# Kernel tuning notes

Hardware: AMD Instinct MI355X
Metric: run time of the kernel (lower is better)

The kernel has to match this reference:

```python
import jax, jax.numpy as jnp
import numpy as np

B, T, D_IN, UNITS = 64, 512, 1024, 1024


def setup_inputs() -> dict:
    key = jax.random.key(0)
    k1, k2, k3 = jax.random.split(key, 3)
    x = jax.random.normal(k1, (B, T, D_IN), dtype=jnp.float32)
    kernel = jax.random.normal(k2, (D_IN, UNITS), dtype=jnp.float32) * (1.0 / np.sqrt(D_IN))
    recurrent_kernel = jax.random.normal(k3, (UNITS, UNITS), dtype=jnp.float32) * (1.0 / np.sqrt(UNITS))
    return {"x": x, "kernel": kernel, "recurrent_kernel": recurrent_kernel}


def reference(x, kernel, recurrent_kernel):
    # Hoist input-to-hidden projection out of the time loop: [B,T,U]
    xk = jnp.einsum('btd,du->btu', x, kernel)

    def step(h, xk_t):
        # Elman step: h' = relu(x_t @ W + h @ U)
        h_new = jax.nn.relu(xk_t + h @ recurrent_kernel)
        return h_new, h_new

    h0 = jnp.zeros((x.shape[0], kernel.shape[1]), dtype=x.dtype)
    _, outs = jax.lax.scan(step, h0, jnp.swapaxes(xk, 0, 1))  # outs: [T,B,U]
    return jnp.swapaxes(outs, 0, 1)  # [B,T,U]
```

## Files before the change

kernel.cpp:

```cpp
#include <hip/hip_runtime.h>
#include <cstdint>
#include <cstddef>


typedef __attribute__((ext_vector_type(8))) short short8;
typedef __attribute__((ext_vector_type(4))) float f32x4;

static __device__ __forceinline__ unsigned short f2bf_rne(float f) {
  unsigned u = __float_as_uint(f);
  u += 0x7fffu + ((u >> 16) & 1u);
  return (unsigned short)(u >> 16);
}

static __device__ __forceinline__ void st_g16_cc(unsigned short* p, unsigned short val) {
  unsigned v32 = val;
  asm volatile("global_store_short %0, %1, off sc0 sc1"
               :: "v"(p), "v"(v32) : "memory");
}
static __device__ __forceinline__ void wait_vm0() {
  asm volatile("s_waitcnt vmcnt(0)" ::: "memory");
}
static __device__ __forceinline__ unsigned ld_flag_cc(const unsigned int* p) {
  unsigned v;
  asm volatile("global_load_dword %0, %1, off sc0 sc1\n\t"
               "s_waitcnt vmcnt(0)"
               : "=v"(v) : "v"(p) : "memory");
  return v;
}
static __device__ __forceinline__ void flag_add_cc(unsigned int* p, unsigned val) {
  asm volatile("global_atomic_add %0, %1, off sc1"
               :: "v"(p), "v"(val) : "memory");
}

__global__ __launch_bounds__(256) void xproj_kernel(const float* __restrict__ x,
                                                    const float* __restrict__ kern,
                                                    float* __restrict__ out) {
  __shared__ unsigned short Abuf[128 * 40];
  __shared__ unsigned short Bbuf[128 * 40];
  const int tid = threadIdx.x;
  const int lane = tid & 63;
  const int wv = tid >> 6;
  const int q = lane >> 4;
  const int lr = lane & 15;
  const int wm = (wv >> 1) * 64;
  const int wn = (wv & 1) * 64;
  const long rowbase = (long)blockIdx.y * 128;
  const int colbase = blockIdx.x * 128;

  f32x4 acc[4][4];
#pragma unroll
  for (int i = 0; i < 4; i++)
#pragma unroll
    for (int j = 0; j < 4; j++) acc[i][j] = (f32x4)0.f;

  for (int kb = 0; kb < 1024; kb += 32) {
#pragma unroll
    for (int r = 0; r < 4; ++r) {
      int idx = tid + r * 256;
      int m = idx >> 3;
      int kk = (idx & 7) * 4;
      float4 v = *(const float4*)(x + (rowbase + m) * 1024 + kb + kk);
      ushort4 w4;
      w4.x = f2bf_rne(v.x); w4.y = f2bf_rne(v.y);
      w4.z = f2bf_rne(v.z); w4.w = f2bf_rne(v.w);
      *(ushort4*)&Abuf[m * 40 + kk] = w4;
    }
#pragma unroll
    for (int r = 0; r < 4; ++r) {
      int idx = tid + r * 256;
      int kr = idx >> 5;
      int nn = (idx & 31) * 4;
      float4 v = *(const float4*)(kern + (long)(kb + kr) * 1024 + colbase + nn);
      Bbuf[(nn + 0) * 40 + kr] = f2bf_rne(v.x);
      Bbuf[(nn + 1) * 40 + kr] = f2bf_rne(v.y);
      Bbuf[(nn + 2) * 40 + kr] = f2bf_rne(v.z);
      Bbuf[(nn + 3) * 40 + kr] = f2bf_rne(v.w);
    }
    __syncthreads();
    short8 af[4], bfr[4];
#pragma unroll
    for (int i = 0; i < 4; i++)
      af[i] = *(const short8*)&Abuf[(wm + i * 16 + lr) * 40 + q * 8];
#pragma unroll
    for (int j = 0; j < 4; j++)
      bfr[j] = *(const short8*)&Bbuf[(wn + j * 16 + lr) * 40 + q * 8];
#pragma unroll
    for (int i = 0; i < 4; i++)
#pragma unroll
      for (int j = 0; j < 4; j++)
        acc[i][j] = __builtin_amdgcn_mfma_f32_16x16x32_bf16(af[i], bfr[j], acc[i][j], 0, 0, 0);
    __syncthreads();
  }
#pragma unroll
  for (int i = 0; i < 4; i++) {
#pragma unroll
    for (int r = 0; r < 4; r++) {
      long row = rowbase + wm + i * 16 + q * 4 + r;
      float* op = out + row * 1024 + colbase + wn + lr;
#pragma unroll
      for (int j = 0; j < 4; j++) op[j * 16] = acc[i][j][r];
    }
  }
}

__global__ __launch_bounds__(256) void rnn_scan_kernel(const float* __restrict__ R,
                                                       float* __restrict__ out,
                                                       unsigned short* __restrict__ hbuf,
                                                       unsigned int* __restrict__ flags) {
  const int tid = threadIdx.x;
  const int lane = tid & 63;
  const int wv = tid >> 6;
  const int q = lane >> 4;
  const int lr = lane & 15;
  const int cluster = blockIdx.x & 3;
  const int cg = blockIdx.x >> 2;

  short8 w[2][8];
#pragma unroll
  for (int nt = 0; nt < 2; nt++) {
    int col = cg * 32 + nt * 16 + lr;
#pragma unroll
    for (int cc = 0; cc < 8; cc++) {
      int k0 = wv * 256 + cc * 32 + q * 8;
      short8 t8;
#pragma unroll
      for (int j = 0; j < 8; j++)
        t8[j] = (short)f2bf_rne(R[(long)(k0 + j) * 1024 + col]);
      w[nt][cc] = t8;
    }
  }

  __shared__ float red[4 * 2 * 64 * 4];
  unsigned int* myflag = flags + cluster * 64;
  const int m_lo = tid >> 5;
  const int myn = tid & 31;
  const int off0 = (wv * 32 + q) * 128 + lr * 8;

  for (int t = 0; t < 512; ++t) {
    f32x4 acc0 = (f32x4)0.f, acc1 = (f32x4)0.f;
    if (t > 0) {
      const unsigned short* hb = hbuf + (size_t)((((t - 1) & 1) * 2 + 0) * 4 + cluster) * 16384;
      const unsigned short* lb = hbuf + (size_t)((((t - 1) & 1) * 2 + 1) * 4 + cluster) * 16384;
      const unsigned short* a0 = hb + off0;
      const unsigned short* a4 = a0 + 2048;
      const unsigned short* b0 = lb + off0;
      const unsigned short* b4 = b0 + 2048;
      short8 ah[8], al[8];
      asm volatile(
          "global_load_dwordx4 %0,  %16, off sc0 sc1\n\t"
          "global_load_dwordx4 %1,  %16, off offset:1024 sc0 sc1\n\t"
          "global_load_dwordx4 %2,  %16, off offset:2048 sc0 sc1\n\t"
          "global_load_dwordx4 %3,  %16, off offset:3072 sc0 sc1\n\t"
          "global_load_dwordx4 %4,  %17, off sc0 sc1\n\t"
          "global_load_dwordx4 %5,  %17, off offset:1024 sc0 sc1\n\t"
          "global_load_dwordx4 %6,  %17, off offset:2048 sc0 sc1\n\t"
          "global_load_dwordx4 %7,  %17, off offset:3072 sc0 sc1\n\t"
          "global_load_dwordx4 %8,  %18, off sc0 sc1\n\t"
          "global_load_dwordx4 %9,  %18, off offset:1024 sc0 sc1\n\t"
          "global_load_dwordx4 %10, %18, off offset:2048 sc0 sc1\n\t"
          "global_load_dwordx4 %11, %18, off offset:3072 sc0 sc1\n\t"
          "global_load_dwordx4 %12, %19, off sc0 sc1\n\t"
          "global_load_dwordx4 %13, %19, off offset:1024 sc0 sc1\n\t"
          "global_load_dwordx4 %14, %19, off offset:2048 sc0 sc1\n\t"
          "global_load_dwordx4 %15, %19, off offset:3072 sc0 sc1\n\t"
          "s_waitcnt vmcnt(0)"
          : "=&v"(ah[0]), "=&v"(ah[1]), "=&v"(ah[2]), "=&v"(ah[3]),
            "=&v"(ah[4]), "=&v"(ah[5]), "=&v"(ah[6]), "=&v"(ah[7]),
            "=&v"(al[0]), "=&v"(al[1]), "=&v"(al[2]), "=&v"(al[3]),
            "=&v"(al[4]), "=&v"(al[5]), "=&v"(al[6]), "=&v"(al[7])
          : "v"(a0), "v"(a4), "v"(b0), "v"(b4)
          : "memory");
#pragma unroll
      for (int cc = 0; cc < 8; cc++) {
        acc0 = __builtin_amdgcn_mfma_f32_16x16x32_bf16(ah[cc], w[0][cc], acc0, 0, 0, 0);
        acc0 = __builtin_amdgcn_mfma_f32_16x16x32_bf16(al[cc], w[0][cc], acc0, 0, 0, 0);
        acc1 = __builtin_amdgcn_mfma_f32_16x16x32_bf16(ah[cc], w[1][cc], acc1, 0, 0, 0);
        acc1 = __builtin_amdgcn_mfma_f32_16x16x32_bf16(al[cc], w[1][cc], acc1, 0, 0, 0);
      }
    }
    *(f32x4*)&red[((wv * 2 + 0) * 64 + lane) * 4] = acc0;
    *(f32x4*)&red[((wv * 2 + 1) * 64 + lane) * 4] = acc1;
    __syncthreads();
#pragma unroll
    for (int mi = 0; mi < 2; ++mi) {
      int m = m_lo + mi * 8;
      int nt = myn >> 4;
      int ln = (myn & 15) + ((m >> 2) & 3) * 16;
      int r = m & 3;
      float s = red[((0 * 2 + nt) * 64 + ln) * 4 + r] + red[((1 * 2 + nt) * 64 + ln) * 4 + r] +
                red[((2 * 2 + nt) * 64 + ln) * 4 + r] + red[((3 * 2 + nt) * 64 + ln) * 4 + r];
      long orow = (long)(cluster * 16 + m) * 512 + t;
      float* op = out + orow * 1024 + cg * 32 + myn;
      float h = s + *op;
      h = fmaxf(h, 0.0f);
      *op = h;
      unsigned short hi = f2bf_rne(h);
      float hf = __uint_as_float(((unsigned)hi) << 16);
      unsigned short lo = f2bf_rne(h - hf);
      int k = cg * 32 + myn;
      int off = (k >> 3) * 128 + m * 8 + (k & 7);
      st_g16_cc(hbuf + (size_t)(((t & 1) * 2 + 0) * 4 + cluster) * 16384 + off, hi);
      st_g16_cc(hbuf + (size_t)(((t & 1) * 2 + 1) * 4 + cluster) * 16384 + off, lo);
    }
    if (t < 511) {
      wait_vm0();
      __syncthreads();
      if (tid == 0) {
        flag_add_cc(myflag, 1u);
        unsigned target = 32u * (unsigned)(t + 1);
        while (ld_flag_cc(myflag) < target) {
          __builtin_amdgcn_s_sleep(1);
        }
      }
      __syncthreads();
    }
  }
}

extern "C" void kernel_launch(void* const* d_in, const int* in_sizes, int n_in,
                              void* d_out, int out_size, void* d_ws, size_t ws_size,
                              hipStream_t stream) {
  const float* x = (const float*)d_in[0];
  const float* kern = (const float*)d_in[1];
  const float* R = (const float*)d_in[2];
  float* out = (float*)d_out;

  unsigned short* hbuf = (unsigned short*)d_ws;
  unsigned int* flags = (unsigned int*)((char*)d_ws + (size_t)2 * 2 * 4 * 16384 * sizeof(unsigned short));
  hipMemsetAsync(flags, 0, 1024, stream);

  dim3 g1(8, 256), b1(256);
  xproj_kernel<<<g1, b1, 0, stream>>>(x, kern, out);
  rnn_scan_kernel<<<128, 256, 0, stream>>>(R, out, hbuf, flags);
}
```

Before: 2.287 ms.

## Restructure recurrent scan into 32 wide blocks with per-wave flag barrier

The scan kernel now launches 32 blocks of 512 threads, each owning 128 output columns with 8 waves splitting K, instead of 128 blocks of 256 threads. The single atomic-counter barrier becomes per-wave monotonic flag stores, polled by a whole wave through a ballot, so waves no longer serialize on thread 0 and two __syncthreads. It also prefetches the xk value, packs the hidden-state stores into 64-bit writes, and overlaps the low-part loads with the high-part MFMAs. The costs are a larger 8-way LDS reduction, more weight registers per thread, and correctness that depends on the flag ordering.

After: 5.029 ms. 120% more time.

```diff
diff --git a/kernel.cpp b/kernel.cpp
--- a/kernel.cpp
+++ b/kernel.cpp
@@ -12,11 +12,6 @@
   return (unsigned short)(u >> 16);
 }
 
-static __device__ __forceinline__ void st_g16_cc(unsigned short* p, unsigned short val) {
-  unsigned v32 = val;
-  asm volatile("global_store_short %0, %1, off sc0 sc1"
-               :: "v"(p), "v"(v32) : "memory");
-}
 static __device__ __forceinline__ void wait_vm0() {
   asm volatile("s_waitcnt vmcnt(0)" ::: "memory");
 }
@@ -27,9 +22,13 @@
                : "=v"(v) : "v"(p) : "memory");
   return v;
 }
-static __device__ __forceinline__ void flag_add_cc(unsigned int* p, unsigned val) {
-  asm volatile("global_atomic_add %0, %1, off sc1"
-               :: "v"(p), "v"(val) : "memory");
+static __device__ __forceinline__ void st_flag_cc(unsigned int* p, unsigned v) {
+  asm volatile("global_store_dword %0, %1, off sc0 sc1"
+               :: "v"(p), "v"(v) : "memory");
+}
+static __device__ __forceinline__ void st_g64_cc(unsigned short* p, unsigned long long v) {
+  asm volatile("global_store_dwordx2 %0, %1, off sc0 sc1"
+               :: "v"(p), "v"(v) : "memory");
 }
 
 __global__ __launch_bounds__(256) void xproj_kernel(const float* __restrict__ x,
@@ -103,10 +102,10 @@
   }
 }
 
-__global__ __launch_bounds__(256) void rnn_scan_kernel(const float* __restrict__ R,
-                                                       float* __restrict__ out,
-                                                       unsigned short* __restrict__ hbuf,
-                                                       unsigned int* __restrict__ flags) {
+__global__ __launch_bounds__(512, 2) void rnn_scan_kernel(const float* __restrict__ R,
+                                                          float* __restrict__ out,
+                                                          unsigned short* __restrict__ hbuf,
+                                                          unsigned int* __restrict__ flags) {
   const int tid = threadIdx.x;
   const int lane = tid & 63;
   const int wv = tid >> 6;
@@ -114,14 +113,15 @@
   const int lr = lane & 15;
   const int cluster = blockIdx.x & 3;
   const int cg = blockIdx.x >> 2;
-
-  short8 w[2][8];
-#pragma unroll
-  for (int nt = 0; nt < 2; nt++) {
-    int col = cg * 32 + nt * 16 + lr;
-#pragma unroll
-    for (int cc = 0; cc < 8; cc++) {
-      int k0 = wv * 256 + cc * 32 + q * 8;
+  const int colbase = cg * 128;
+
+  short8 w[8][4];
+#pragma unroll
+  for (int nt = 0; nt < 8; nt++) {
+    const int col = colbase + nt * 16 + lr;
+#pragma unroll
+    for (int cc = 0; cc < 4; cc++) {
+      const int k0 = wv * 128 + cc * 32 + q * 8;
       short8 t8;
 #pragma unroll
       for (int j = 0; j < 8; j++)
@@ -130,90 +130,96 @@
     }
   }
 
-  __shared__ float red[4 * 2 * 64 * 4];
-  unsigned int* myflag = flags + cluster * 64;
-  const int m_lo = tid >> 5;
-  const int myn = tid & 31;
-  const int off0 = (wv * 32 + q) * 128 + lr * 8;
+  __shared__ float red[8 * 8 * 64 * 4];
+
+  const int m = tid >> 5;
+  const int cw0 = (tid & 31) * 4;
+  const int kglob = colbase + cw0;
+  const int hoff = (kglob >> 3) * 128 + m * 8 + (kglob & 7);
+  const int off0 = (wv * 16 + q) * 128 + lr * 8;
+  const int ntr = cw0 >> 4;
+  const int Lb = (cw0 & 15) + ((m >> 2) << 4);
+  const int rr = m & 3;
+
+  unsigned int* myflags = flags + cluster * 64;
+  unsigned int* myflag = myflags + cg * 8 + wv;
+  float* myout = out + ((long)(cluster * 16 + m) * 512) * 1024 + kglob;
 
   for (int t = 0; t < 512; ++t) {
-    f32x4 acc0 = (f32x4)0.f, acc1 = (f32x4)0.f;
+    const float4 xkv = *(const float4*)(myout + (long)t * 1024);
+    f32x4 acc[8];
+#pragma unroll
+    for (int nt = 0; nt < 8; nt++) acc[nt] = (f32x4)0.f;
+
     if (t > 0) {
-      const unsigned short* hb = hbuf + (size_t)((((t - 1) & 1) * 2 + 0) * 4 + cluster) * 16384;
-      const unsigned short* lb = hbuf + (size_t)((((t - 1) & 1) * 2 + 1) * 4 + cluster) * 16384;
-      const unsigned short* a0 = hb + off0;
-      const unsigned short* a4 = a0 + 2048;
-      const unsigned short* b0 = lb + off0;
-      const unsigned short* b4 = b0 + 2048;
-      short8 ah[8], al[8];
+      const unsigned target = (unsigned)t;
+      unsigned f = ld_flag_cc(myflags + lane);
+      while (__ballot(f < target) != 0ull) {
+        f = ld_flag_cc(myflags + lane);
+      }
+      const unsigned short* a0 =
+          hbuf + (size_t)((((t - 1) & 1) * 2 + 0) * 4 + cluster) * 16384 + off0;
+      const unsigned short* b0 =
+          hbuf + (size_t)((((t - 1) & 1) * 2 + 1) * 4 + cluster) * 16384 + off0;
+      short8 ah[4], al[4];
       asm volatile(
-          "global_load_dwordx4 %0,  %16, off sc0 sc1\n\t"
-          "global_load_dwordx4 %1,  %16, off offset:1024 sc0 sc1\n\t"
-          "global_load_dwordx4 %2,  %16, off offset:2048 sc0 sc1\n\t"
-          "global_load_dwordx4 %3,  %16, off offset:3072 sc0 sc1\n\t"
-          "global_load_dwordx4 %4,  %17, off sc0 sc1\n\t"
-          "global_load_dwordx4 %5,  %17, off offset:1024 sc0 sc1\n\t"
-          "global_load_dwordx4 %6,  %17, off offset:2048 sc0 sc1\n\t"
-          "global_load_dwordx4 %7,  %17, off offset:3072 sc0 sc1\n\t"
-          "global_load_dwordx4 %8,  %18, off sc0 sc1\n\t"
-          "global_load_dwordx4 %9,  %18, off offset:1024 sc0 sc1\n\t"
-          "global_load_dwordx4 %10, %18, off offset:2048 sc0 sc1\n\t"
-          "global_load_dwordx4 %11, %18, off offset:3072 sc0 sc1\n\t"
-          "global_load_dwordx4 %12, %19, off sc0 sc1\n\t"
-          "global_load_dwordx4 %13, %19, off offset:1024 sc0 sc1\n\t"
-          "global_load_dwordx4 %14, %19, off offset:2048 sc0 sc1\n\t"
-          "global_load_dwordx4 %15, %19, off offset:3072 sc0 sc1\n\t"
-          "s_waitcnt vmcnt(0)"
+          "global_load_dwordx4 %0, %8, off sc0 sc1\n\t"
+          "global_load_dwordx4 %1, %8, off offset:1024 sc0 sc1\n\t"
+          "global_load_dwordx4 %2, %8, off offset:2048 sc0 sc1\n\t"
+          "global_load_dwordx4 %3, %8, off offset:3072 sc0 sc1\n\t"
+          "global_load_dwordx4 %4, %9, off sc0 sc1\n\t"
+          "global_load_dwordx4 %5, %9, off offset:1024 sc0 sc1\n\t"
+          "global_load_dwordx4 %6, %9, off offset:2048 sc0 sc1\n\t"
+          "global_load_dwordx4 %7, %9, off offset:3072 sc0 sc1\n\t"
+          "s_waitcnt vmcnt(4)"
           : "=&v"(ah[0]), "=&v"(ah[1]), "=&v"(ah[2]), "=&v"(ah[3]),
-            "=&v"(ah[4]), "=&v"(ah[5]), "=&v"(ah[6]), "=&v"(ah[7]),
-            "=&v"(al[0]), "=&v"(al[1]), "=&v"(al[2]), "=&v"(al[3]),
-            "=&v"(al[4]), "=&v"(al[5]), "=&v"(al[6]), "=&v"(al[7])
-          : "v"(a0), "v"(a4), "v"(b0), "v"(b4)
+            "=&v"(al[0]), "=&v"(al[1]), "=&v"(al[2]), "=&v"(al[3])
+          : "v"(a0), "v"(b0)
           : "memory");
 #pragma unroll
-      for (int cc = 0; cc < 8; cc++) {
-        acc0 = __builtin_amdgcn_mfma_f32_16x16x32_bf16(ah[cc], w[0][cc], acc0, 0, 0, 0);
-        acc0 = __builtin_amdgcn_mfma_f32_16x16x32_bf16(al[cc], w[0][cc], acc0, 0, 0, 0);
-        acc1 = __builtin_amdgcn_mfma_f32_16x16x32_bf16(ah[cc], w[1][cc], acc1, 0, 0, 0);
-        acc1 = __builtin_amdgcn_mfma_f32_16x16x32_bf16(al[cc], w[1][cc], acc1, 0, 0, 0);
-      }
-    }
-    *(f32x4*)&red[((wv * 2 + 0) * 64 + lane) * 4] = acc0;
-    *(f32x4*)&red[((wv * 2 + 1) * 64 + lane) * 4] = acc1;
+      for (int cc = 0; cc < 4; cc++)
+#pragma unroll
+        for (int nt = 0; nt < 8; nt++)
+          acc[nt] = __builtin_amdgcn_mfma_f32_16x16x32_bf16(ah[cc], w[nt][cc], acc[nt], 0, 0, 0);
+      asm volatile("s_waitcnt vmcnt(0)"
+                   : "+v"(al[0]), "+v"(al[1]), "+v"(al[2]), "+v"(al[3])
+                   :: "memory");
+#pragma unroll
+      for (int cc = 0; cc < 4; cc++)
+#pragma unroll
+        for (int nt = 0; nt < 8; nt++)
+          acc[nt] = __builtin_amdgcn_mfma_f32_16x16x32_bf16(al[cc], w[nt][cc], acc[nt], 0, 0, 0);
+    }
+
+#pragma unroll
+    for (int nt = 0; nt < 8; nt++)
+      *(f32x4*)&red[((wv * 8 + nt) * 64 + lane) * 4] = acc[nt];
     __syncthreads();
-#pragma unroll
-    for (int mi = 0; mi < 2; ++mi) {
-      int m = m_lo + mi * 8;
-      int nt = myn >> 4;
-      int ln = (myn & 15) + ((m >> 2) & 3) * 16;
-      int r = m & 3;
-      float s = red[((0 * 2 + nt) * 64 + ln) * 4 + r] + red[((1 * 2 + nt) * 64 + ln) * 4 + r] +
-                red[((2 * 2 + nt) * 64 + ln) * 4 + r] + red[((3 * 2 + nt) * 64 + ln) * 4 + r];
-      long orow = (long)(cluster * 16 + m) * 512 + t;
-      float* op = out + orow * 1024 + cg * 32 + myn;
-      float h = s + *op;
-      h = fmaxf(h, 0.0f);
-      *op = h;
+
+    const float xarr[4] = {xkv.x, xkv.y, xkv.z, xkv.w};
+    float hv[4];
+    unsigned long long hpk = 0ull, lpk = 0ull;
+#pragma unroll
+    for (int j = 0; j < 4; ++j) {
+      float s = 0.f;
+#pragma unroll
+      for (int kq = 0; kq < 8; ++kq)
+        s += red[((kq * 8 + ntr) * 64 + Lb + j) * 4 + rr];
+      float h = fmaxf(s + xarr[j], 0.0f);
+      hv[j] = h;
       unsigned short hi = f2bf_rne(h);
       float hf = __uint_as_float(((unsigned)hi) << 16);
       unsigned short lo = f2bf_rne(h - hf);
-      int k = cg * 32 + myn;
-      int off = (k >> 3) * 128 + m * 8 + (k & 7);
-      st_g16_cc(hbuf + (size_t)(((t & 1) * 2 + 0) * 4 + cluster) * 16384 + off, hi);
-      st_g16_cc(hbuf + (size_t)(((t & 1) * 2 + 1) * 4 + cluster) * 16384 + off, lo);
-    }
-    if (t < 511) {
-      wait_vm0();
-      __syncthreads();
-      if (tid == 0) {
-        flag_add_cc(myflag, 1u);
-        unsigned target = 32u * (unsigned)(t + 1);
-        while (ld_flag_cc(myflag) < target) {
-          __builtin_amdgcn_s_sleep(1);
-        }
-      }
-      __syncthreads();
-    }
+      hpk |= (unsigned long long)hi << (16 * j);
+      lpk |= (unsigned long long)lo << (16 * j);
+    }
+    st_g64_cc(hbuf + (size_t)(((t & 1) * 2 + 0) * 4 + cluster) * 16384 + hoff, hpk);
+    st_g64_cc(hbuf + (size_t)(((t & 1) * 2 + 1) * 4 + cluster) * 16384 + hoff, lpk);
+    wait_vm0();
+    if (lane == 0) st_flag_cc(myflag, (unsigned)(t + 1));
+    float4 hq;
+    hq.x = hv[0]; hq.y = hv[1]; hq.z = hv[2]; hq.w = hv[3];
+    *(float4*)(myout + (long)t * 1024) = hq;
   }
 }
 
@@ -231,5 +237,5 @@
 
   dim3 g1(8, 256), b1(256);
   xproj_kernel<<<g1, b1, 0, stream>>>(x, kern, out);
-  rnn_scan_kernel<<<128, 256, 0, stream>>>(R, out, hbuf, flags);
-}
+  rnn_scan_kernel<<<32, 512, 0, stream>>>(R, out, hbuf, flags);
+}
```

## Replace atomic flag barrier with tag-embedded data polling and fewer larger scan blocks

Applied to the files above, without the earlier changes.

Removes the per-step global atomic counter barrier. Consumers now spin-load the hidden-state buffer until the sign bits of the bf16 hi words match an expected step tag, so the data itself acts as the ready signal. The scan uses 32 blocks of 512 threads, each owning 128 columns, instead of 128 blocks of 256. This cuts the number of participants per cluster and lets each block write packed 16-byte hi/lo units. The tag lives in the sign bit of the hi bf16, which is valid only because ReLU outputs are non-negative. Polling re-reads the whole tile and relies on the visibility order of the 16-byte stores.

Measured after the change: 2.401 ms. 5.0% more time.

```diff
diff --git a/kernel.cpp b/kernel.cpp
--- a/kernel.cpp
+++ b/kernel.cpp
@@ -5,31 +5,12 @@
 
 typedef __attribute__((ext_vector_type(8))) short short8;
 typedef __attribute__((ext_vector_type(4))) float f32x4;
+typedef __attribute__((ext_vector_type(4))) unsigned int u32x4;
 
 static __device__ __forceinline__ unsigned short f2bf_rne(float f) {
   unsigned u = __float_as_uint(f);
   u += 0x7fffu + ((u >> 16) & 1u);
   return (unsigned short)(u >> 16);
-}
-
-static __device__ __forceinline__ void st_g16_cc(unsigned short* p, unsigned short val) {
-  unsigned v32 = val;
-  asm volatile("global_store_short %0, %1, off sc0 sc1"
-               :: "v"(p), "v"(v32) : "memory");
-}
-static __device__ __forceinline__ void wait_vm0() {
-  asm volatile("s_waitcnt vmcnt(0)" ::: "memory");
-}
-static __device__ __forceinline__ unsigned ld_flag_cc(const unsigned int* p) {
-  unsigned v;
-  asm volatile("global_load_dword %0, %1, off sc0 sc1\n\t"
-               "s_waitcnt vmcnt(0)"
-               : "=v"(v) : "v"(p) : "memory");
-  return v;
-}
-static __device__ __forceinline__ void flag_add_cc(unsigned int* p, unsigned val) {
-  asm volatile("global_atomic_add %0, %1, off sc1"
-               :: "v"(p), "v"(val) : "memory");
 }
 
 __global__ __launch_bounds__(256) void xproj_kernel(const float* __restrict__ x,
@@ -103,10 +84,9 @@
   }
 }
 
-__global__ __launch_bounds__(256) void rnn_scan_kernel(const float* __restrict__ R,
-                                                       float* __restrict__ out,
-                                                       unsigned short* __restrict__ hbuf,
-                                                       unsigned int* __restrict__ flags) {
+__global__ __launch_bounds__(512, 2) void rnn_scan_kernel(const float* __restrict__ R,
+                                                          float* __restrict__ out,
+                                                          unsigned char* __restrict__ hbuf) {
   const int tid = threadIdx.x;
   const int lane = tid & 63;
   const int wv = tid >> 6;
@@ -114,14 +94,17 @@
   const int lr = lane & 15;
   const int cluster = blockIdx.x & 3;
   const int cg = blockIdx.x >> 2;
-
-  short8 w[2][8];
-#pragma unroll
-  for (int nt = 0; nt < 2; nt++) {
-    int col = cg * 32 + nt * 16 + lr;
+  const int ks = wv & 3;
+  const int nh = wv >> 2;
+  const int colbase = cg * 128;
+
+  short8 w[4][8];
+#pragma unroll
+  for (int nt = 0; nt < 4; nt++) {
+    const int col = colbase + nh * 64 + nt * 16 + lr;
 #pragma unroll
     for (int cc = 0; cc < 8; cc++) {
-      int k0 = wv * 256 + cc * 32 + q * 8;
+      const int k0 = ks * 256 + cc * 32 + q * 8;
       short8 t8;
 #pragma unroll
       for (int j = 0; j < 8; j++)
@@ -130,90 +113,137 @@
     }
   }
 
-  __shared__ float red[4 * 2 * 64 * 4];
-  unsigned int* myflag = flags + cluster * 64;
-  const int m_lo = tid >> 5;
-  const int myn = tid & 31;
-  const int off0 = (wv * 32 + q) * 128 + lr * 8;
+  __shared__ float red[32 * 264];
+  __shared__ float xbuf[16 * 132];
+
+  const int nw = tid & 127;
+  const int mg = tid >> 7;
+  const int kglob = colbase + nw;
+  const int ntr = nw >> 4;
+  const int rlane = mg * 16 + (nw & 15);
+  const int pm = tid & 15;
+  const int pkq = tid >> 4;
+  const size_t punit = (size_t)((cg * 32 + pkq) * 16 + pm) * 16;
+  const size_t cbase = (size_t)ks * 16384 + q * 512 + lr * 16;
+
+  float* opb0 = out + ((long)(cluster * 16 + mg * 4 + 0) * 512) * 1024 + kglob;
+  float* opb1 = out + ((long)(cluster * 16 + mg * 4 + 1) * 512) * 1024 + kglob;
+  float* opb2 = out + ((long)(cluster * 16 + mg * 4 + 2) * 512) * 1024 + kglob;
+  float* opb3 = out + ((long)(cluster * 16 + mg * 4 + 3) * 512) * 1024 + kglob;
 
   for (int t = 0; t < 512; ++t) {
-    f32x4 acc0 = (f32x4)0.f, acc1 = (f32x4)0.f;
+    const long tOff = (long)t * 1024;
+    const float xk0 = opb0[tOff];
+    const float xk1 = opb1[tOff];
+    const float xk2 = opb2[tOff];
+    const float xk3 = opb3[tOff];
+
+    f32x4 acc[4];
+#pragma unroll
+    for (int nt = 0; nt < 4; nt++) acc[nt] = (f32x4)0.f;
+
     if (t > 0) {
-      const unsigned short* hb = hbuf + (size_t)((((t - 1) & 1) * 2 + 0) * 4 + cluster) * 16384;
-      const unsigned short* lb = hbuf + (size_t)((((t - 1) & 1) * 2 + 1) * 4 + cluster) * 16384;
-      const unsigned short* a0 = hb + off0;
-      const unsigned short* a4 = a0 + 2048;
-      const unsigned short* b0 = lb + off0;
-      const unsigned short* b4 = b0 + 2048;
-      short8 ah[8], al[8];
-      asm volatile(
-          "global_load_dwordx4 %0,  %16, off sc0 sc1\n\t"
-          "global_load_dwordx4 %1,  %16, off offset:1024 sc0 sc1\n\t"
-          "global_load_dwordx4 %2,  %16, off offset:2048 sc0 sc1\n\t"
-          "global_load_dwordx4 %3,  %16, off offset:3072 sc0 sc1\n\t"
-          "global_load_dwordx4 %4,  %17, off sc0 sc1\n\t"
-          "global_load_dwordx4 %5,  %17, off offset:1024 sc0 sc1\n\t"
-          "global_load_dwordx4 %6,  %17, off offset:2048 sc0 sc1\n\t"
-          "global_load_dwordx4 %7,  %17, off offset:3072 sc0 sc1\n\t"
-          "global_load_dwordx4 %8,  %18, off sc0 sc1\n\t"
-          "global_load_dwordx4 %9,  %18, off offset:1024 sc0 sc1\n\t"
-          "global_load_dwordx4 %10, %18, off offset:2048 sc0 sc1\n\t"
-          "global_load_dwordx4 %11, %18, off offset:3072 sc0 sc1\n\t"
-          "global_load_dwordx4 %12, %19, off sc0 sc1\n\t"
-          "global_load_dwordx4 %13, %19, off offset:1024 sc0 sc1\n\t"
-          "global_load_dwordx4 %14, %19, off offset:2048 sc0 sc1\n\t"
-          "global_load_dwordx4 %15, %19, off offset:3072 sc0 sc1\n\t"
-          "s_waitcnt vmcnt(0)"
-          : "=&v"(ah[0]), "=&v"(ah[1]), "=&v"(ah[2]), "=&v"(ah[3]),
-            "=&v"(ah[4]), "=&v"(ah[5]), "=&v"(ah[6]), "=&v"(ah[7]),
-            "=&v"(al[0]), "=&v"(al[1]), "=&v"(al[2]), "=&v"(al[3]),
-            "=&v"(al[4]), "=&v"(al[5]), "=&v"(al[6]), "=&v"(al[7])
-          : "v"(a0), "v"(a4), "v"(b0), "v"(b4)
-          : "memory");
+      const unsigned tag = ((unsigned)(t - 1) >> 1) & 15u;
+      const unsigned E0 = ((tag & 1u) << 15) | (((tag >> 1) & 1u) << 31);
+      const unsigned E1 = (((tag >> 2) & 1u) << 15) | (((tag >> 3) & 1u) << 31);
+      const unsigned char* blk =
+          hbuf + (size_t)(((t - 1) & 1) * 4 + cluster) * 65536 + cbase;
+      const unsigned char* b0 = blk;
+      const unsigned char* b1 = blk + 4096;
+      const unsigned char* b2 = blk + 8192;
+      const unsigned char* b3 = blk + 12288;
+      u32x4 U[16];
+      for (;;) {
+        asm volatile(
+            "global_load_dwordx4 %0,  %16, off sc0 sc1\n\t"
+            "global_load_dwordx4 %1,  %16, off offset:256 sc0 sc1\n\t"
+            "global_load_dwordx4 %2,  %16, off offset:2048 sc0 sc1\n\t"
+            "global_load_dwordx4 %3,  %16, off offset:2304 sc0 sc1\n\t"
+            "global_load_dwordx4 %4,  %17, off sc0 sc1\n\t"
+            "global_load_dwordx4 %5,  %17, off offset:256 sc0 sc1\n\t"
+            "global_load_dwordx4 %6,  %17, off offset:2048 sc0 sc1\n\t"
+            "global_load_dwordx4 %7,  %17, off offset:2304 sc0 sc1\n\t"
+            "global_load_dwordx4 %8,  %18, off sc0 sc1\n\t"
+            "global_load_dwordx4 %9,  %18, off offset:256 sc0 sc1\n\t"
+            "global_load_dwordx4 %10, %18, off offset:2048 sc0 sc1\n\t"
+            "global_load_dwordx4 %11, %18, off offset:2304 sc0 sc1\n\t"
+            "global_load_dwordx4 %12, %19, off sc0 sc1\n\t"
+            "global_load_dwordx4 %13, %19, off offset:256 sc0 sc1\n\t"
+            "global_load_dwordx4 %14, %19, off offset:2048 sc0 sc1\n\t"
+            "global_load_dwordx4 %15, %19, off offset:2304 sc0 sc1\n\t"
+            "s_waitcnt vmcnt(0)"
+            : "=&v"(U[0]), "=&v"(U[1]), "=&v"(U[2]), "=&v"(U[3]),
+              "=&v"(U[4]), "=&v"(U[5]), "=&v"(U[6]), "=&v"(U[7]),
+              "=&v"(U[8]), "=&v"(U[9]), "=&v"(U[10]), "=&v"(U[11]),
+              "=&v"(U[12]), "=&v"(U[13]), "=&v"(U[14]), "=&v"(U[15])
+            : "v"(b0), "v"(b1), "v"(b2), "v"(b3)
+            : "memory");
+        unsigned bad = 0u;
+#pragma unroll
+        for (int i = 0; i < 16; i++)
+          bad |= ((U[i][0] ^ E0) | (U[i][1] ^ E1)) & 0x80008000u;
+        if (__ballot(bad != 0u) == 0ull) break;
+      }
 #pragma unroll
       for (int cc = 0; cc < 8; cc++) {
-        acc0 = __builtin_amdgcn_mfma_f32_16x16x32_bf16(ah[cc], w[0][cc], acc0, 0, 0, 0);
-        acc0 = __builtin_amdgcn_mfma_f32_16x16x32_bf16(al[cc], w[0][cc], acc0, 0, 0, 0);
-        acc1 = __builtin_amdgcn_mfma_f32_16x16x32_bf16(ah[cc], w[1][cc], acc1, 0, 0, 0);
-        acc1 = __builtin_amdgcn_mfma_f32_16x16x32_bf16(al[cc], w[1][cc], acc1, 0, 0, 0);
-      }
-    }
-    *(f32x4*)&red[((wv * 2 + 0) * 64 + lane) * 4] = acc0;
-    *(f32x4*)&red[((wv * 2 + 1) * 64 + lane) * 4] = acc1;
-    __syncthreads();
-#pragma unroll
-    for (int mi = 0; mi < 2; ++mi) {
-      int m = m_lo + mi * 8;
-      int nt = myn >> 4;
-      int ln = (myn & 15) + ((m >> 2) & 3) * 16;
-      int r = m & 3;
-      float s = red[((0 * 2 + nt) * 64 + ln) * 4 + r] + red[((1 * 2 + nt) * 64 + ln) * 4 + r] +
-                red[((2 * 2 + nt) * 64 + ln) * 4 + r] + red[((3 * 2 + nt) * 64 + ln) * 4 + r];
-      long orow = (long)(cluster * 16 + m) * 512 + t;
-      float* op = out + orow * 1024 + cg * 32 + myn;
-      float h = s + *op;
-      h = fmaxf(h, 0.0f);
-      *op = h;
-      unsigned short hi = f2bf_rne(h);
-      float hf = __uint_as_float(((unsigned)hi) << 16);
-      unsigned short lo = f2bf_rne(h - hf);
-      int k = cg * 32 + myn;
-      int off = (k >> 3) * 128 + m * 8 + (k & 7);
-      st_g16_cc(hbuf + (size_t)(((t & 1) * 2 + 0) * 4 + cluster) * 16384 + off, hi);
-      st_g16_cc(hbuf + (size_t)(((t & 1) * 2 + 1) * 4 + cluster) * 16384 + off, lo);
-    }
-    if (t < 511) {
-      wait_vm0();
-      __syncthreads();
-      if (tid == 0) {
-        flag_add_cc(myflag, 1u);
-        unsigned target = 32u * (unsigned)(t + 1);
-        while (ld_flag_cc(myflag) < target) {
-          __builtin_amdgcn_s_sleep(1);
+        const int i0 = (cc >> 1) * 4 + (cc & 1) * 2;
+        u32x4 hivec, lovec;
+        hivec[0] = U[i0][0] & 0x7fff7fffu;
+        hivec[1] = U[i0][1] & 0x7fff7fffu;
+        hivec[2] = U[i0 + 1][0] & 0x7fff7fffu;
+        hivec[3] = U[i0 + 1][1] & 0x7fff7fffu;
+        lovec[0] = U[i0][2];
+        lovec[1] = U[i0][3];
+        lovec[2] = U[i0 + 1][2];
+        lovec[3] = U[i0 + 1][3];
+        short8 ah = *(short8*)&hivec;
+        short8 al = *(short8*)&lovec;
+#pragma unroll
+        for (int nt = 0; nt < 4; nt++) {
+          acc[nt] = __builtin_amdgcn_mfma_f32_16x16x32_bf16(ah, w[nt][cc], acc[nt], 0, 0, 0);
+          acc[nt] = __builtin_amdgcn_mfma_f32_16x16x32_bf16(al, w[nt][cc], acc[nt], 0, 0, 0);
         }
       }
-      __syncthreads();
-    }
+    }
+
+#pragma unroll
+    for (int nt = 0; nt < 4; nt++)
+      *(f32x4*)&red[(ks * 8 + nh * 4 + nt) * 264 + lane * 4] = acc[nt];
+    __syncthreads();
+    f32x4 s = *(const f32x4*)&red[(0 * 8 + ntr) * 264 + rlane * 4];
+#pragma unroll
+    for (int kq = 1; kq < 4; ++kq)
+      s += *(const f32x4*)&red[(kq * 8 + ntr) * 264 + rlane * 4];
+
+    const float xarr[4] = {xk0, xk1, xk2, xk3};
+    float hv[4];
+#pragma unroll
+    for (int r = 0; r < 4; ++r) hv[r] = fmaxf(s[r] + xarr[r], 0.0f);
+    opb0[tOff] = hv[0];
+    opb1[tOff] = hv[1];
+    opb2[tOff] = hv[2];
+    opb3[tOff] = hv[3];
+#pragma unroll
+    for (int r = 0; r < 4; ++r) xbuf[(mg * 4 + r) * 132 + nw] = hv[r];
+    __syncthreads();
+    const f32x4 v = *(const f32x4*)&xbuf[pm * 132 + pkq * 4];
+    const unsigned ptag = ((unsigned)t >> 1) & 15u;
+    unsigned hw[4], lw[4];
+#pragma unroll
+    for (int j = 0; j < 4; ++j) {
+      unsigned short hr = f2bf_rne(v[j]);
+      float hf = __uint_as_float(((unsigned)hr) << 16);
+      hw[j] = (unsigned)hr | (((ptag >> j) & 1u) << 15);
+      lw[j] = (unsigned)f2bf_rne(v[j] - hf);
+    }
+    u32x4 pk;
+    pk[0] = hw[0] | (hw[1] << 16);
+    pk[1] = hw[2] | (hw[3] << 16);
+    pk[2] = lw[0] | (lw[1] << 16);
+    pk[3] = lw[2] | (lw[3] << 16);
+    unsigned char* pst = hbuf + (size_t)((t & 1) * 4 + cluster) * 65536 + punit;
+    asm volatile("global_store_dwordx4 %0, %1, off sc0 sc1"
+                 :: "v"(pst), "v"(pk) : "memory");
   }
 }
 
@@ -225,11 +255,10 @@
   const float* R = (const float*)d_in[2];
   float* out = (float*)d_out;
 
-  unsigned short* hbuf = (unsigned short*)d_ws;
-  unsigned int* flags = (unsigned int*)((char*)d_ws + (size_t)2 * 2 * 4 * 16384 * sizeof(unsigned short));
-  hipMemsetAsync(flags, 0, 1024, stream);
+  unsigned char* hbuf = (unsigned char*)d_ws;
+  hipMemsetAsync(hbuf, 0xFF, (size_t)2 * 4 * 65536, stream);
 
   dim3 g1(8, 256), b1(256);
   xproj_kernel<<<g1, b1, 0, stream>>>(x, kern, out);
-  rnn_scan_kernel<<<128, 256, 0, stream>>>(R, out, hbuf, flags);
-}
+  rnn_scan_kernel<<<32, 512, 0, stream>>>(R, out, hbuf);
+}
```
